# Performance work log

Measured on AMD Instinct MI355X. Metric: run time of the kernel, lower is better.

Reference implementation:

```python
import jax, jax.numpy as jnp
import numpy as np

K = 16

def _pairwise_sqdist(a, b):
    # a:[B,n,3] b:[B,m,3] -> [B,n,m]
    return (jnp.sum(a * a, -1)[:, :, None] + jnp.sum(b * b, -1)[:, None, :]
            - 2.0 * jnp.einsum('bnd,bmd->bnm', a, b))

def _group(x, idx):
    # x:[B,N,C], idx:[B,M,K] -> [B,M,K,C]
    return jax.vmap(lambda xb, ib: xb[ib])(x, idx)

def _gather(x, idx):
    # x:[B,N,C], idx:[B,M] -> [B,M,C]
    return jax.vmap(lambda xb, ib: xb[ib])(x, idx)

def _knn_idx(pos, k):
    p = jax.lax.stop_gradient(pos)
    d = _pairwise_sqdist(p, p)
    return jax.lax.top_k(-d, k)[1]

def _leaky(v):
    return jnp.where(v >= 0, v, 0.2 * v)

def _edge_conv(x, pos, w_self, w_edge, idx=None):
    if idx is None:
        idx = _knn_idx(pos, K)
    nx = _group(x, idx)                      # [B,N,K,C]
    npos = _group(pos, idx)                  # [B,N,K,3]
    rel = pos[:, :, None, :] - npos
    d2 = jnp.sum(rel * rel, -1, keepdims=True)
    h = jnp.concatenate([nx, rel, d2], -1)   # [B,N,K,C+4]
    term_n = jnp.mean(h @ w_edge, axis=2)
    return _leaky(x @ w_self + term_n)

def _fps(pos, npoint):
    # furthest point sampling, starts at index 0 (matches pointnet2 CUDA op)
    pos = jax.lax.stop_gradient(pos)
    B, N, _ = pos.shape
    def body(carry, _):
        dists, far = carry
        c = jnp.take_along_axis(pos, far[:, None, None], axis=1)  # [B,1,3]
        d = jnp.sum((pos - c) ** 2, -1)
        dists = jnp.minimum(dists, d)
        return (dists, jnp.argmax(dists, axis=1).astype(jnp.int32)), far
    init = (jnp.full((B, N), 1e10, pos.dtype), jnp.zeros((B,), jnp.int32))
    _, idxs = jax.lax.scan(body, init, None, length=npoint)
    return jnp.transpose(idxs)  # [B,npoint]

def _three_nn(unknown, known):
    d = _pairwise_sqdist(unknown, known)
    negd, idx = jax.lax.top_k(-d, 3)
    dist = jnp.maximum(-negd, 0.0)  # squared dists, as in pointnet2 kernel
    return jax.lax.stop_gradient(dist), idx  # three_nn is non-differentiable

def _interp_weights(dist):
    recip = 1.0 / (dist + 1e-8)
    return recip / jnp.sum(recip, axis=2, keepdims=True)

def _three_interp(feat, idx, weight):
    g = _group(feat, idx)  # [B,n,3,C]
    return jnp.sum(weight[..., None] * g, axis=2)

def _forward(x, pos, w_self0, w_edge0, w_self1, w_edge1, w_self2, w_edge2,
             w_up1, b_up1, w_upc1_self, w_upc1_edge,
             w_up0, b_up0, w_upc0_self, w_upc0_edge, w_out, b_out):
    feat0 = _edge_conv(x, pos, w_self0, w_edge0)
    pos0 = pos
    n1 = pos0.shape[1] // 2
    idx1 = _fps(pos0, n1)
    pos1 = _gather(pos0, idx1)
    feat1 = _edge_conv(_gather(feat0, idx1), pos1, w_self1, w_edge1)
    n2 = pos1.shape[1] // 2
    idx2 = _fps(pos1, n2)
    pos2 = _gather(pos1, idx2)
    feat2 = _edge_conv(_gather(feat1, idx2), pos2, w_self2, w_edge2)
    dist, idx = _three_nn(pos1, pos2)
    w = _interp_weights(dist)
    cat1 = jnp.concatenate([_three_interp(feat2, idx, w), feat1], -1)
    feat_up1 = _leaky(cat1 @ w_up1 + b_up1)
    feat_up1 = _edge_conv(feat_up1, pos1, w_upc1_self, w_upc1_edge)
    dist, idx = _three_nn(pos0, pos1)
    w = _interp_weights(dist)
    cat0 = jnp.concatenate([_three_interp(feat_up1, idx, w), feat0], -1)
    feat_up0 = _leaky(cat0 @ w_up0 + b_up0)
    feat_out = _edge_conv(feat_up0, pos0, w_upc0_self, w_upc0_edge)
    return feat_out @ w_out + b_out

def setup_inputs() -> dict:
    B, N, CIN, D = 2, 8192, 4, 64
    key = jax.random.key(0)
    ks = jax.random.split(key, 20)
    def w(k, fin, fout):
        return jax.random.normal(k, (fin, fout), jnp.float32) / np.sqrt(fin)
    return {
        'x': jax.random.normal(ks[0], (B, N, CIN), jnp.float32),
        'pos': jax.random.normal(ks[1], (B, N, 3), jnp.float32),
        'w_self0': w(ks[2], CIN, D),        'w_edge0': w(ks[3], CIN + 4, D),
        'w_self1': w(ks[4], D, 2 * D),      'w_edge1': w(ks[5], D + 4, 2 * D),
        'w_self2': w(ks[6], 2 * D, 4 * D),  'w_edge2': w(ks[7], 2 * D + 4, 4 * D),
        'w_up1': w(ks[8], 6 * D, 2 * D),    'b_up1': jnp.zeros((2 * D,), jnp.float32),
        'w_upc1_self': w(ks[9], 2 * D, 2 * D), 'w_upc1_edge': w(ks[10], 2 * D + 4, 2 * D),
        'w_up0': w(ks[11], 3 * D, D),       'b_up0': jnp.zeros((D,), jnp.float32),
        'w_upc0_self': w(ks[12], D, D),     'w_upc0_edge': w(ks[13], D + 4, D),
        'w_out': w(ks[14], D, 128),         'b_out': jnp.zeros((128,), jnp.float32),
    }

def reference(x, pos, w_self0, w_edge0, w_self1, w_edge1, w_self2, w_edge2,
              w_up1, b_up1, w_upc1_self, w_upc1_edge,
              w_up0, b_up0, w_upc0_self, w_upc0_edge, w_out, b_out):
    return _forward(x, pos, w_self0, w_edge0, w_self1, w_edge1, w_self2, w_edge2,
                    w_up1, b_up1, w_upc1_self, w_upc1_edge,
                    w_up0, b_up0, w_upc0_self, w_upc0_edge, w_out, b_out)
```

## Files before the change

kernel.cpp:

```cpp
#include <hip/hip_runtime.h>
#include <cstdint>

typedef unsigned long long u64;

static __device__ __forceinline__ float leakyf(float v) { return v >= 0.f ? v : 0.2f * v; }

__global__ void pack_kernel(const float* __restrict__ pos, int total, float4* __restrict__ out)
{
  int i = blockIdx.x * 256 + threadIdx.x;
  if (i >= total) return;
  float x = pos[i*3+0], y = pos[i*3+1], z = pos[i*3+2];
  out[i] = make_float4(x, y, z, (x*x + y*y) + z*z);
}

template<int CTRL>
static __device__ __forceinline__ float dpp_max_f_step(float x)
{
  int y = __builtin_amdgcn_update_dpp(__float_as_int(x), __float_as_int(x), CTRL, 0xF, 0xF, false);
  return fmaxf(x, __int_as_float(y));
}
static __device__ __forceinline__ float wave64_max_f(float x)
{
  x = dpp_max_f_step<0x111>(x);
  x = dpp_max_f_step<0x112>(x);
  x = dpp_max_f_step<0x114>(x);
  x = dpp_max_f_step<0x118>(x);
  x = dpp_max_f_step<0x142>(x);
  x = dpp_max_f_step<0x143>(x);
  return __int_as_float(__builtin_amdgcn_readlane(__float_as_int(x), 63));
}
template<int CTRL>
static __device__ __forceinline__ unsigned dpp_max_u_step(unsigned x)
{
  unsigned y = (unsigned)__builtin_amdgcn_update_dpp((int)x, (int)x, CTRL, 0xF, 0xF, false);
  return x > y ? x : y;
}
static __device__ __forceinline__ unsigned wave64_max_u(unsigned x)
{
  x = dpp_max_u_step<0x111>(x);
  x = dpp_max_u_step<0x112>(x);
  x = dpp_max_u_step<0x114>(x);
  x = dpp_max_u_step<0x118>(x);
  x = dpp_max_u_step<0x142>(x);
  x = dpp_max_u_step<0x143>(x);
  return (unsigned)__builtin_amdgcn_readlane((int)x, 63);
}

template<int N, int NPOINT>
__global__ __launch_bounds__(512) void fps_kernel(const float* __restrict__ pos,
                                                  int* __restrict__ out_idx,
                                                  float* __restrict__ out_pos,
                                                  float4* __restrict__ out_pp)
{
  constexpr int BLOCK = 512;
  constexpr int NPT = N / BLOCK;
  const int b = blockIdx.x;
  const float* P = pos + (size_t)b * N * 3;
  int* oi = out_idx + (size_t)b * NPOINT;
  float* op = out_pos + (size_t)b * NPOINT * 3;
  float4* opp = out_pp + (size_t)b * NPOINT;

  __shared__ float4 spos[N];
  __shared__ u64 redk[2][8];

  const int t = threadIdx.x;
  const int lane = t & 63;
  const int wv = t >> 6;

  float px[NPT], py[NPT], pz[NPT], dist[NPT];
  unsigned iv[NPT];
#pragma unroll
  for (int j = 0; j < NPT; ++j) {
    int i = t + j * BLOCK;
    float x = P[i*3+0], y = P[i*3+1], z = P[i*3+2];
    spos[i] = make_float4(x, y, z, (x*x + y*y) + z*z);
    px[j] = x; py[j] = y; pz[j] = z; dist[j] = 1e10f;
    iv[j] = 0xFFFFFFFFu - (unsigned)i;
  }
  if (t == 0) oi[0] = 0;
  __syncthreads();

  int far = 0;
  for (int it = 1; it < NPOINT; ++it) {
    const float4 c = spos[far];
    if (t == ((it - 1) & (BLOCK - 1))) {
      op[(it-1)*3+0] = c.x; op[(it-1)*3+1] = c.y; op[(it-1)*3+2] = c.z;
      opp[it-1] = c;
    }
    float bd = -1.f; unsigned biv = 0u;
#pragma unroll
    for (int j = 0; j < NPT; ++j) {
      float dx = px[j] - c.x, dy = py[j] - c.y, dz = pz[j] - c.z;
      float d  = fmaf(dz, dz, fmaf(dy, dy, dx * dx));
      float nd = fminf(dist[j], d);
      dist[j] = nd;
      bool bt = nd > bd;
      bd  = bt ? nd : bd;
      biv = bt ? iv[j] : biv;
    }
    const float wmax = wave64_max_f(bd);
    const unsigned cand = (bd == wmax) ? biv : 0u;
    const unsigned wiv = wave64_max_u(cand);
    const int par = it & 1;
    if (lane == 0) redk[par][wv] = ((u64)__float_as_uint(wmax) << 32) | (u64)wiv;
    __syncthreads();
    u64 key = ((u64)__float_as_uint(wmax) << 32) | (u64)wiv;
#pragma unroll
    for (int w2 = 0; w2 < 8; ++w2) {
      u64 o = redk[par][w2];
      if (o > key) key = o;
    }
    far = (int)(0xFFFFFFFFu - (unsigned)(key & 0xFFFFFFFFull));
    if (t == 0) oi[it] = far;
  }
  {
    const float4 c = spos[far];
    if (t == ((NPOINT - 1) & (BLOCK - 1))) {
      op[(NPOINT-1)*3+0] = c.x; op[(NPOINT-1)*3+1] = c.y; op[(NPOINT-1)*3+2] = c.z;
      opp[NPOINT-1] = c;
    }
  }
}

template<int G>
__global__ __launch_bounds__(256) void knn_kernel(const float4* __restrict__ pp, int M,
                                                  int* __restrict__ out)
{
  const int b = blockIdx.y;
  const float4* P = pp + (size_t)b * M;
  const int tid = threadIdx.x;
  constexpr int QPB = 256 / G;
  const int q = blockIdx.x * QPB + tid / G;
  const int seg = tid % G;

  __shared__ float4 tile[512];

  const float4 qp = P[q];
  const float qx = qp.x, qy = qp.y, qz = qp.z, qq = qp.w;

  float a[16]; int id[16];
#pragma unroll
  for (int j = 0; j < 16; ++j) { a[j] = 3.4e38f; id[j] = 0x7fffffff; }

  for (int t0 = 0; t0 < M; t0 += 512) {
    __syncthreads();
    tile[tid]       = P[t0 + tid];
    tile[tid + 256] = P[t0 + tid + 256];
    __syncthreads();
#pragma unroll 4
    for (int i = seg; i < 512; i += G) {
      float4 c = tile[i];
      float d = (qq + c.w) - 2.f * ((qx*c.x + qy*c.y) + qz*c.z);
      int gi = t0 + i;
      if (d < a[15]) {
        bool cc[16];
#pragma unroll
        for (int j = 0; j < 16; ++j) cc[j] = d < a[j];
#pragma unroll
        for (int j = 15; j >= 1; --j) {
          a[j]  = cc[j-1] ? a[j-1]  : (cc[j] ? d  : a[j]);
          id[j] = cc[j-1] ? id[j-1] : (cc[j] ? gi : id[j]);
        }
        if (cc[0]) { a[0] = d; id[0] = gi; }
      }
    }
  }
#pragma unroll
  for (int s = G/2; s >= 1; s >>= 1) {
    float bd[16]; int bi[16];
#pragma unroll
    for (int j = 0; j < 16; ++j) { bd[j] = __shfl_xor(a[j], s); bi[j] = __shfl_xor(id[j], s); }
#pragma unroll
    for (int j = 0; j < 16; ++j) {
      float od = bd[15-j]; int ob = bi[15-j];
      bool take = (od < a[j]) || (od == a[j] && ob < id[j]);
      a[j]  = take ? od : a[j];
      id[j] = take ? ob : id[j];
    }
#pragma unroll
    for (int st = 8; st >= 1; st >>= 1) {
#pragma unroll
      for (int j = 0; j < 16; ++j) {
        if ((j & st) == 0) {
          const int j2 = j + st;
          bool sw = (a[j2] < a[j]) || (a[j2] == a[j] && id[j2] < id[j]);
          float lod = sw ? a[j2] : a[j];  int loi = sw ? id[j2] : id[j];
          float hid = sw ? a[j]  : a[j2]; int hii = sw ? id[j]  : id[j2];
          a[j] = lod; id[j] = loi; a[j2] = hid; id[j2] = hii;
        }
      }
    }
  }
  if (seg == 0) {
    int* opp = out + ((size_t)b * M + q) * 16;
#pragma unroll
    for (int j = 0; j < 16; ++j) opp[j] = id[j];
  }
}

template<int G>
__global__ __launch_bounds__(256) void three_nn_kernel(const float4* __restrict__ qpp,
                                                       const float4* __restrict__ kpp,
                                                       int Mq, int Mk,
                                                       int* __restrict__ oidx, float* __restrict__ ow)
{
  const int b = blockIdx.y;
  const float4* Q  = qpp + (size_t)b * Mq;
  const float4* Kp = kpp + (size_t)b * Mk;
  const int tid = threadIdx.x;
  constexpr int QPB = 256 / G;
  const int q = blockIdx.x * QPB + tid / G;
  const int seg = tid % G;

  __shared__ float4 tile[512];

  const float4 qp = Q[q];
  const float qx = qp.x, qy = qp.y, qz = qp.z, qq = qp.w;

  float a[4]; int id[4];
#pragma unroll
  for (int j = 0; j < 4; ++j) { a[j] = 3.4e38f; id[j] = 0x7fffffff; }

  for (int t0 = 0; t0 < Mk; t0 += 512) {
    __syncthreads();
    tile[tid]       = Kp[t0 + tid];
    tile[tid + 256] = Kp[t0 + tid + 256];
    __syncthreads();
#pragma unroll 4
    for (int i = seg; i < 512; i += G) {
      float4 c = tile[i];
      float d = (qq + c.w) - 2.f * ((qx*c.x + qy*c.y) + qz*c.z);
      int gi = t0 + i;
      if (d < a[3]) {
        bool c0 = d < a[0], c1 = d < a[1], c2 = d < a[2];
        a[3]  = c2 ? a[2]  : d;                id[3] = c2 ? id[2] : gi;
        a[2]  = c1 ? a[1]  : (c2 ? d  : a[2]); id[2] = c1 ? id[1] : (c2 ? gi : id[2]);
        a[1]  = c0 ? a[0]  : (c1 ? d  : a[1]); id[1] = c0 ? id[0] : (c1 ? gi : id[1]);
        if (c0) { a[0] = d; id[0] = gi; }
      }
    }
  }
#pragma unroll
  for (int s = G/2; s >= 1; s >>= 1) {
    float bd[4]; int bi[4];
#pragma unroll
    for (int j = 0; j < 4; ++j) { bd[j] = __shfl_xor(a[j], s); bi[j] = __shfl_xor(id[j], s); }
#pragma unroll
    for (int j = 0; j < 4; ++j) {
      float od = bd[3-j]; int ob = bi[3-j];
      bool take = (od < a[j]) || (od == a[j] && ob < id[j]);
      a[j]  = take ? od : a[j];
      id[j] = take ? ob : id[j];
    }
#pragma unroll
    for (int st = 2; st >= 1; st >>= 1) {
#pragma unroll
      for (int j = 0; j < 4; ++j) {
        if ((j & st) == 0) {
          const int j2 = j + st;
          bool sw = (a[j2] < a[j]) || (a[j2] == a[j] && id[j2] < id[j]);
          float lod = sw ? a[j2] : a[j];  int loi = sw ? id[j2] : id[j];
          float hid = sw ? a[j]  : a[j2]; int hii = sw ? id[j]  : id[j2];
          a[j] = lod; id[j] = loi; a[j2] = hid; id[j2] = hii;
        }
      }
    }
  }
  if (seg == 0) {
    float d0 = fmaxf(a[0], 0.f), d1 = fmaxf(a[1], 0.f), d2 = fmaxf(a[2], 0.f);
    float r0 = 1.f/(d0 + 1e-8f), r1 = 1.f/(d1 + 1e-8f), r2 = 1.f/(d2 + 1e-8f);
    float s = (r0 + r1) + r2;
    size_t o = ((size_t)b * Mq + q) * 3;
    oidx[o+0] = id[0]; oidx[o+1] = id[1]; oidx[o+2] = id[2];
    ow[o+0] = r0/s; ow[o+1] = r1/s; ow[o+2] = r2/s;
  }
}

__global__ void hbar_kernel(const float* __restrict__ x, const float* __restrict__ pos,
                            const int* __restrict__ idx, int Mlvl, int C, int B,
                            float* __restrict__ out)
{
  const int Ct = C + 4;
  const int tot = B * Mlvl * Ct;
  int e = blockIdx.x * 256 + threadIdx.x;
  if (e >= tot) return;
  const int c  = e % Ct;
  const int p  = e / Ct;
  const int b  = p / Mlvl;
  const int lm = p % Mlvl;
  const int* ip = idx + (size_t)p * 16;
  float s = 0.f;
  if (c < C) {
    const float* xb = x + (size_t)b * Mlvl * C;
#pragma unroll 4
    for (int k = 0; k < 16; ++k) s += xb[(size_t)ip[k] * C + c];
  } else if (c < C + 3) {
    const int dd = c - C;
    const float* pb = pos + (size_t)b * Mlvl * 3;
    const float pc = pb[lm*3 + dd];
#pragma unroll 4
    for (int k = 0; k < 16; ++k) s += pc - pb[ip[k]*3 + dd];
  } else {
    const float* pb = pos + (size_t)b * Mlvl * 3;
    const float px = pb[lm*3+0], py = pb[lm*3+1], pz = pb[lm*3+2];
#pragma unroll 4
    for (int k = 0; k < 16; ++k) {
      int n = ip[k];
      float dx = px - pb[n*3+0], dy = py - pb[n*3+1], dz = pz - pb[n*3+2];
      s += (dx*dx + dy*dy) + dz*dz;
    }
  }
  out[e] = s * 0.0625f;
}

__global__ void interp_kernel(const float* __restrict__ f, const int* __restrict__ nidx,
                              const float* __restrict__ nw, int Mq, int Msub, int C, int B,
                              float* __restrict__ out)
{
  const int tot = B * Mq * C;
  int e = blockIdx.x * 256 + threadIdx.x;
  if (e >= tot) return;
  const int c = e % C;
  const int p = e / C;
  const int b = p / Mq;
  const float* fb = f + (size_t)b * Msub * C;
  const int* ip   = nidx + (size_t)p * 3;
  const float* wp = nw   + (size_t)p * 3;
  out[e] = (wp[0] * fb[(size_t)ip[0]*C + c] + wp[1] * fb[(size_t)ip[1]*C + c])
         +  wp[2] * fb[(size_t)ip[2]*C + c];
}

__global__ void gather_kernel(const float* __restrict__ src, const int* __restrict__ idx,
                              int Mq, int Msrc, int C, int B, float* __restrict__ dst)
{
  const int tot = B * Mq * C;
  int e = blockIdx.x * 256 + threadIdx.x;
  if (e >= tot) return;
  const int c = e % C;
  const int p = e / C;
  const int b = p / Mq;
  dst[e] = src[((size_t)b * Msrc + idx[p]) * C + c];
}

__global__ __launch_bounds__(256) void gemm_kernel(const float* __restrict__ A, int Ka,
                                                   const float* __restrict__ B2, int Kb,
                                                   const float* __restrict__ W1,
                                                   const float* __restrict__ W2,
                                                   const float* __restrict__ bias,
                                                   float* __restrict__ out,
                                                   int M, int F, int act)
{
  __shared__ __align__(16) float As[16][64];
  __shared__ __align__(16) float Ws[16][64];
  const int tid  = threadIdx.x;
  const int row0 = blockIdx.x * 64;
  const int col0 = blockIdx.y * 64;
  const int tx = tid & 15, ty = tid >> 4;
  const int K = Ka + Kb;
  float acc[4][4] = {};
  for (int k0 = 0; k0 < K; k0 += 16) {
#pragma unroll
    for (int i = 0; i < 4; ++i) {
      int e = tid + i * 256;
      int m = e & 63, kk = e >> 6;
      int k = k0 + kk;
      float v = 0.f;
      if (k < Ka)     v = A [(size_t)(row0 + m) * Ka + k];
      else if (k < K) v = B2[(size_t)(row0 + m) * Kb + (k - Ka)];
      As[kk][m] = v;
      float wv = 0.f;
      if (k < Ka)     wv = W1[(size_t)k * F + col0 + m];
      else if (k < K) wv = W2[(size_t)(k - Ka) * F + col0 + m];
      Ws[kk][m] = wv;
    }
    __syncthreads();
#pragma unroll
    for (int kk = 0; kk < 16; ++kk) {
      const float4 a4 = *reinterpret_cast<const float4*>(&As[kk][ty * 4]);
      const float4 b4 = *reinterpret_cast<const float4*>(&Ws[kk][tx * 4]);
      const float av[4] = {a4.x, a4.y, a4.z, a4.w};
      const float bv[4] = {b4.x, b4.y, b4.z, b4.w};
#pragma unroll
      for (int i2 = 0; i2 < 4; ++i2)
#pragma unroll
        for (int j2 = 0; j2 < 4; ++j2)
          acc[i2][j2] = fmaf(av[i2], bv[j2], acc[i2][j2]);
    }
    __syncthreads();
  }
#pragma unroll
  for (int i2 = 0; i2 < 4; ++i2) {
    int r = row0 + ty * 4 + i2;
#pragma unroll
    for (int j2 = 0; j2 < 4; ++j2) {
      int cc = col0 + tx * 4 + j2;
      float v = acc[i2][j2];
      if (bias) v += bias[cc];
      if (act)  v = leakyf(v);
      out[(size_t)r * F + cc] = v;
    }
  }
}

extern "C" void kernel_launch(void* const* d_in, const int* in_sizes, int n_in,
                              void* d_out, int out_size, void* d_ws, size_t ws_size,
                              hipStream_t stream)
{
  (void)in_sizes; (void)n_in; (void)out_size; (void)ws_size;
  const float* x          = (const float*)d_in[0];
  const float* pos        = (const float*)d_in[1];
  const float* w_self0    = (const float*)d_in[2];
  const float* w_edge0    = (const float*)d_in[3];
  const float* w_self1    = (const float*)d_in[4];
  const float* w_edge1    = (const float*)d_in[5];
  const float* w_self2    = (const float*)d_in[6];
  const float* w_edge2    = (const float*)d_in[7];
  const float* w_up1      = (const float*)d_in[8];
  const float* b_up1      = (const float*)d_in[9];
  const float* w_upc1s    = (const float*)d_in[10];
  const float* w_upc1e    = (const float*)d_in[11];
  const float* w_up0      = (const float*)d_in[12];
  const float* b_up0      = (const float*)d_in[13];
  const float* w_upc0s    = (const float*)d_in[14];
  const float* w_upc0e    = (const float*)d_in[15];
  const float* w_out      = (const float*)d_in[16];
  const float* b_out      = (const float*)d_in[17];
  float* out = (float*)d_out;

  char* ws = (char*)d_ws;
  size_t off = 0;
  auto alloc = [&](size_t nbytes) -> void* {
    off = (off + 255) & ~(size_t)255;
    void* p = ws + off;
    off += nbytes;
    return p;
  };
  int*    knn0   = (int*)   alloc((size_t)2*8192*16*4);
  int*    knn1   = (int*)   alloc((size_t)2*4096*16*4);
  int*    knn2   = (int*)   alloc((size_t)2*2048*16*4);
  int*    idx1   = (int*)   alloc((size_t)2*4096*4);
  int*    idx2   = (int*)   alloc((size_t)2*2048*4);
  float*  pos1   = (float*) alloc((size_t)2*4096*3*4);
  float*  pos2   = (float*) alloc((size_t)2*2048*3*4);
  float4* pp0    = (float4*)alloc((size_t)2*8192*16);
  float4* pp1    = (float4*)alloc((size_t)2*4096*16);
  float4* pp2    = (float4*)alloc((size_t)2*2048*16);
  float*  feat0  = (float*) alloc((size_t)2*8192*64*4);
  float*  feat0g = (float*) alloc((size_t)2*4096*64*4);
  float*  feat1  = (float*) alloc((size_t)2*4096*128*4);
  float*  feat1g = (float*) alloc((size_t)2*2048*128*4);
  float*  feat2  = (float*) alloc((size_t)2*2048*256*4);
  int*    nn1i   = (int*)   alloc((size_t)2*4096*3*4);
  float*  nn1w   = (float*) alloc((size_t)2*4096*3*4);
  int*    nn0i   = (int*)   alloc((size_t)2*8192*3*4);
  float*  nn0w   = (float*) alloc((size_t)2*8192*3*4);
  float*  interp = (float*) alloc((size_t)2*4096*256*4);
  float*  hbar   = (float*) alloc((size_t)2*8192*68*4);
  float*  fupa   = (float*) alloc((size_t)2*4096*128*4);
  float*  fup1   = (float*) alloc((size_t)2*4096*128*4);
  float*  fout   = (float*) alloc((size_t)2*8192*64*4);

  pack_kernel<<<64, 256, 0, stream>>>(pos, 2*8192, pp0);
  knn_kernel<16><<<dim3(512, 2), 256, 0, stream>>>(pp0, 8192, knn0);
  hbar_kernel<<<512, 256, 0, stream>>>(x, pos, knn0, 8192, 4, 2, hbar);
  gemm_kernel<<<dim3(256, 1), 256, 0, stream>>>(x, 4, hbar, 8, w_self0, w_edge0, nullptr,
                                                feat0, 16384, 64, 1);
  fps_kernel<8192, 4096><<<2, 512, 0, stream>>>(pos, idx1, pos1, pp1);
  gather_kernel<<<2048, 256, 0, stream>>>(feat0, idx1, 4096, 8192, 64, 2, feat0g);
  knn_kernel<16><<<dim3(256, 2), 256, 0, stream>>>(pp1, 4096, knn1);
  hbar_kernel<<<2176, 256, 0, stream>>>(feat0g, pos1, knn1, 4096, 64, 2, hbar);
  gemm_kernel<<<dim3(128, 2), 256, 0, stream>>>(feat0g, 64, hbar, 68, w_self1, w_edge1, nullptr,
                                                feat1, 8192, 128, 1);
  fps_kernel<4096, 2048><<<2, 512, 0, stream>>>(pos1, idx2, pos2, pp2);
  gather_kernel<<<2048, 256, 0, stream>>>(feat1, idx2, 2048, 4096, 128, 2, feat1g);
  knn_kernel<16><<<dim3(128, 2), 256, 0, stream>>>(pp2, 2048, knn2);
  hbar_kernel<<<2112, 256, 0, stream>>>(feat1g, pos2, knn2, 2048, 128, 2, hbar);
  gemm_kernel<<<dim3(64, 4), 256, 0, stream>>>(feat1g, 128, hbar, 132, w_self2, w_edge2, nullptr,
                                               feat2, 4096, 256, 1);
  three_nn_kernel<16><<<dim3(256, 2), 256, 0, stream>>>(pp1, pp2, 4096, 2048, nn1i, nn1w);
  interp_kernel<<<8192, 256, 0, stream>>>(feat2, nn1i, nn1w, 4096, 2048, 256, 2, interp);
  gemm_kernel<<<dim3(128, 2), 256, 0, stream>>>(interp, 256, feat1, 128,
                                                w_up1, w_up1 + (size_t)256 * 128, b_up1,
                                                fupa, 8192, 128, 1);
  hbar_kernel<<<4224, 256, 0, stream>>>(fupa, pos1, knn1, 4096, 128, 2, hbar);
  gemm_kernel<<<dim3(128, 2), 256, 0, stream>>>(fupa, 128, hbar, 132, w_upc1s, w_upc1e, nullptr,
                                                fup1, 8192, 128, 1);
  three_nn_kernel<16><<<dim3(512, 2), 256, 0, stream>>>(pp0, pp1, 8192, 4096, nn0i, nn0w);
  interp_kernel<<<8192, 256, 0, stream>>>(fup1, nn0i, nn0w, 8192, 4096, 128, 2, interp);
  gemm_kernel<<<dim3(256, 1), 256, 0, stream>>>(interp, 128, feat0, 64,
                                                w_up0, w_up0 + (size_t)128 * 64, b_up0,
                                                fupa, 16384, 64, 1);
  hbar_kernel<<<4352, 256, 0, stream>>>(fupa, pos, knn0, 8192, 64, 2, hbar);
  gemm_kernel<<<dim3(256, 1), 256, 0, stream>>>(fupa, 64, hbar, 68, w_upc0s, w_upc0e, nullptr,
                                                fout, 16384, 64, 1);
  gemm_kernel<<<dim3(256, 2), 256, 0, stream>>>(fout, 64, nullptr, 0, w_out, nullptr, b_out,
                                                out, 16384, 128, 0);
}
```

Baseline: 6.657 ms.

## Morton-sort FPS points per thread and skip threads whose bounding sphere cannot change

Adds a prep kernel that computes 30-bit Morton codes for each point cloud and bitonic-sorts them in shared memory. Each FPS thread then owns a spatially coherent cluster of points. It keeps a bounding sphere and an upper bound on its current max distance, and skips the per-point distance update when the new centroid is too far to lower any of its distances. Ties are now broken on index explicitly to keep the argmax identical. This targets the serial FPS loop, which dominates runtime, at the cost of two extra sort kernels and a branch per iteration.

```diff
diff --git a/kernel.cpp b/kernel.cpp
--- a/kernel.cpp
+++ b/kernel.cpp
@@ -46,8 +46,72 @@
   return (unsigned)__builtin_amdgcn_readlane((int)x, 63);
 }
 
+static __device__ __forceinline__ unsigned part1by2(unsigned v)
+{
+  v &= 0x3FFu;
+  v = (v | (v << 16)) & 0x030000FFu;
+  v = (v | (v << 8))  & 0x0300F00Fu;
+  v = (v | (v << 4))  & 0x030C30C3u;
+  v = (v | (v << 2))  & 0x09249249u;
+  return v;
+}
+
+template<int N>
+__global__ __launch_bounds__(512) void fps_prep_kernel(const float* __restrict__ pos,
+                                                       unsigned* __restrict__ sordg)
+{
+  const int b = blockIdx.x;
+  const float* P = pos + (size_t)b * N * 3;
+  unsigned* SORD = sordg + (size_t)b * N;
+
+  __shared__ u64 skey[N];
+  __shared__ float sred[512];
+  const int t = threadIdx.x;
+
+  float mn[3] = {3.4e38f, 3.4e38f, 3.4e38f};
+  float mx[3] = {-3.4e38f, -3.4e38f, -3.4e38f};
+  for (int i = t; i < N; i += 512) {
+    float c3[3] = {P[i*3], P[i*3+1], P[i*3+2]};
+#pragma unroll
+    for (int a = 0; a < 3; ++a) { mn[a] = fminf(mn[a], c3[a]); mx[a] = fmaxf(mx[a], c3[a]); }
+  }
+  float bmin[3], inv[3];
+  for (int a = 0; a < 3; ++a) {
+    sred[t] = mn[a]; __syncthreads();
+    for (int s = 256; s > 0; s >>= 1) { if (t < s) sred[t] = fminf(sred[t], sred[t+s]); __syncthreads(); }
+    bmin[a] = sred[0]; __syncthreads();
+    sred[t] = mx[a]; __syncthreads();
+    for (int s = 256; s > 0; s >>= 1) { if (t < s) sred[t] = fmaxf(sred[t], sred[t+s]); __syncthreads(); }
+    float bmax = sred[0]; __syncthreads();
+    inv[a] = 1023.0f / fmaxf(bmax - bmin[a], 1e-20f);
+  }
+  for (int i = t; i < N; i += 512) {
+    float x = P[i*3], y = P[i*3+1], z = P[i*3+2];
+    unsigned cx = (unsigned)fminf(fmaxf((x - bmin[0]) * inv[0], 0.f), 1023.f);
+    unsigned cy = (unsigned)fminf(fmaxf((y - bmin[1]) * inv[1], 0.f), 1023.f);
+    unsigned cz = (unsigned)fminf(fmaxf((z - bmin[2]) * inv[2], 0.f), 1023.f);
+    unsigned code = part1by2(cx) | (part1by2(cy) << 1) | (part1by2(cz) << 2);
+    skey[i] = ((u64)code << 32) | (unsigned)i;
+  }
+  __syncthreads();
+  for (int k = 2; k <= N; k <<= 1)
+    for (int j = k >> 1; j > 0; j >>= 1) {
+      for (int i = t; i < N; i += 512) {
+        int ixj = i ^ j;
+        if (ixj > i) {
+          u64 a = skey[i], c = skey[ixj];
+          if ((a > c) == ((i & k) == 0)) { skey[i] = c; skey[ixj] = a; }
+        }
+      }
+      __syncthreads();
+    }
+  for (int i = t; i < N; i += 512)
+    SORD[i] = (unsigned)(skey[i] & 0xFFFFFFFFull);
+}
+
 template<int N, int NPOINT>
 __global__ __launch_bounds__(512) void fps_kernel(const float* __restrict__ pos,
+                                                  const unsigned* __restrict__ sordg,
                                                   int* __restrict__ out_idx,
                                                   float* __restrict__ out_pos,
                                                   float4* __restrict__ out_pp)
@@ -56,6 +120,7 @@
   constexpr int NPT = N / BLOCK;
   const int b = blockIdx.x;
   const float* P = pos + (size_t)b * N * 3;
+  const unsigned* SORD = sordg + (size_t)b * N;
   int* oi = out_idx + (size_t)b * NPOINT;
   float* op = out_pos + (size_t)b * NPOINT * 3;
   float4* opp = out_pp + (size_t)b * NPOINT;
@@ -67,18 +132,40 @@
   const int lane = t & 63;
   const int wv = t >> 6;
 
+  for (int i = t; i < N; i += BLOCK) {
+    float x = P[i*3+0], y = P[i*3+1], z = P[i*3+2];
+    spos[i] = make_float4(x, y, z, (x*x + y*y) + z*z);
+  }
+  if (t == 0) oi[0] = 0;
+  __syncthreads();
+
   float px[NPT], py[NPT], pz[NPT], dist[NPT];
   unsigned iv[NPT];
+  float mnx = 3.4e38f, mxx = -3.4e38f, mny = 3.4e38f, mxy = -3.4e38f, mnz = 3.4e38f, mxz = -3.4e38f;
 #pragma unroll
   for (int j = 0; j < NPT; ++j) {
-    int i = t + j * BLOCK;
-    float x = P[i*3+0], y = P[i*3+1], z = P[i*3+2];
-    spos[i] = make_float4(x, y, z, (x*x + y*y) + z*z);
-    px[j] = x; py[j] = y; pz[j] = z; dist[j] = 1e10f;
-    iv[j] = 0xFFFFFFFFu - (unsigned)i;
-  }
-  if (t == 0) oi[0] = 0;
-  __syncthreads();
+    unsigned so = SORD[t * NPT + j];
+    float4 v = spos[so];
+    px[j] = v.x; py[j] = v.y; pz[j] = v.z; dist[j] = 1e10f;
+    iv[j] = 0xFFFFFFFFu - so;
+    mnx = fminf(mnx, v.x); mxx = fmaxf(mxx, v.x);
+    mny = fminf(mny, v.y); mxy = fmaxf(mxy, v.y);
+    mnz = fminf(mnz, v.z); mxz = fmaxf(mxz, v.z);
+  }
+  const float gcx = (mnx + mxx) * 0.5f, gcy = (mny + mxy) * 0.5f, gcz = (mnz + mxz) * 0.5f;
+  float r2 = 0.f;
+#pragma unroll
+  for (int j = 0; j < NPT; ++j) {
+    float dx = px[j] - gcx, dy = py[j] - gcy, dz = pz[j] - gcz;
+    r2 = fmaxf(r2, fmaf(dz, dz, fmaf(dy, dy, dx * dx)));
+  }
+  const float r = sqrtf(r2) * 1.0001f;
+  float bd = 1e10f;
+  unsigned biv = iv[0];
+#pragma unroll
+  for (int j = 1; j < NPT; ++j) biv = iv[j] > biv ? iv[j] : biv;
+  float sb = sqrtf(1e10f) + r;
+  float aux = sb * sb * 1.0002f;
 
   int far = 0;
   for (int it = 1; it < NPOINT; ++it) {
@@ -87,16 +174,22 @@
       op[(it-1)*3+0] = c.x; op[(it-1)*3+1] = c.y; op[(it-1)*3+2] = c.z;
       opp[it-1] = c;
     }
-    float bd = -1.f; unsigned biv = 0u;
-#pragma unroll
-    for (int j = 0; j < NPT; ++j) {
-      float dx = px[j] - c.x, dy = py[j] - c.y, dz = pz[j] - c.z;
-      float d  = fmaf(dz, dz, fmaf(dy, dy, dx * dx));
-      float nd = fminf(dist[j], d);
-      dist[j] = nd;
-      bool bt = nd > bd;
-      bd  = bt ? nd : bd;
-      biv = bt ? iv[j] : biv;
+    const float dxg = c.x - gcx, dyg = c.y - gcy, dzg = c.z - gcz;
+    const float ddg = fmaf(dzg, dzg, fmaf(dyg, dyg, dxg * dxg));
+    if (ddg < aux) {
+      bd = -1.f; biv = 0u;
+#pragma unroll
+      for (int j = 0; j < NPT; ++j) {
+        float dx = px[j] - c.x, dy = py[j] - c.y, dz = pz[j] - c.z;
+        float d  = fmaf(dz, dz, fmaf(dy, dy, dx * dx));
+        float nd = fminf(dist[j], d);
+        dist[j] = nd;
+        bool bt = (nd > bd) || ((nd == bd) && (iv[j] > biv));
+        bd  = bt ? nd : bd;
+        biv = bt ? iv[j] : biv;
+      }
+      float s2 = sqrtf(bd) + r;
+      aux = s2 * s2 * 1.0002f;
     }
     const float wmax = wave64_max_f(bd);
     const unsigned cand = (bd == wmax) ? biv : 0u;
@@ -459,19 +552,23 @@
   float*  fupa   = (float*) alloc((size_t)2*4096*128*4);
   float*  fup1   = (float*) alloc((size_t)2*4096*128*4);
   float*  fout   = (float*) alloc((size_t)2*8192*64*4);
+  unsigned* sord1 = (unsigned*)alloc((size_t)2*8192*4);
+  unsigned* sord2 = (unsigned*)alloc((size_t)2*4096*4);
 
   pack_kernel<<<64, 256, 0, stream>>>(pos, 2*8192, pp0);
+  fps_prep_kernel<8192><<<2, 512, 0, stream>>>(pos, sord1);
   knn_kernel<16><<<dim3(512, 2), 256, 0, stream>>>(pp0, 8192, knn0);
   hbar_kernel<<<512, 256, 0, stream>>>(x, pos, knn0, 8192, 4, 2, hbar);
   gemm_kernel<<<dim3(256, 1), 256, 0, stream>>>(x, 4, hbar, 8, w_self0, w_edge0, nullptr,
                                                 feat0, 16384, 64, 1);
-  fps_kernel<8192, 4096><<<2, 512, 0, stream>>>(pos, idx1, pos1, pp1);
+  fps_kernel<8192, 4096><<<2, 512, 0, stream>>>(pos, sord1, idx1, pos1, pp1);
+  fps_prep_kernel<4096><<<2, 512, 0, stream>>>(pos1, sord2);
   gather_kernel<<<2048, 256, 0, stream>>>(feat0, idx1, 4096, 8192, 64, 2, feat0g);
   knn_kernel<16><<<dim3(256, 2), 256, 0, stream>>>(pp1, 4096, knn1);
   hbar_kernel<<<2176, 256, 0, stream>>>(feat0g, pos1, knn1, 4096, 64, 2, hbar);
   gemm_kernel<<<dim3(128, 2), 256, 0, stream>>>(feat0g, 64, hbar, 68, w_self1, w_edge1, nullptr,
                                                 feat1, 8192, 128, 1);
-  fps_kernel<4096, 2048><<<2, 512, 0, stream>>>(pos1, idx2, pos2, pp2);
+  fps_kernel<4096, 2048><<<2, 512, 0, stream>>>(pos1, sord2, idx2, pos2, pp2);
   gather_kernel<<<2048, 256, 0, stream>>>(feat1, idx2, 2048, 4096, 128, 2, feat1g);
   knn_kernel<16><<<dim3(128, 2), 256, 0, stream>>>(pp2, 2048, knn2);
   hbar_kernel<<<2112, 256, 0, stream>>>(feat1g, pos2, knn2, 2048, 128, 2, hbar);
```

New measurement: 11.12 ms. +67.1%, slower.
